# Performance work log

Hardware: AMD Instinct MI355X
Metric: run time of the kernel (lower is better)

## Reference

```python
import jax, jax.numpy as jnp
import numpy as np

B, E, H, L, V = 128, 1024, 1024, 2, 32001  # vocab = output_size + 1
PAD_IDX = 1000


def gru_cell(x, h, w_ih, w_hh, b_ih, b_hh):
    # PyTorch GRU cell math; gates ordered (r, z, n)
    gi = x @ w_ih.T + b_ih            # [B, 3H]
    gh = h @ w_hh.T + b_hh            # [B, 3H]
    i_r, i_z, i_n = jnp.split(gi, 3, axis=-1)
    h_r, h_z, h_n = jnp.split(gh, 3, axis=-1)
    r = jax.nn.sigmoid(i_r + h_r)
    z = jax.nn.sigmoid(i_z + h_z)
    n = jnp.tanh(i_n + r * h_n)
    return (1.0 - z) * n + z * h


def setup_inputs() -> dict:
    key = jax.random.key(0)
    ks = jax.random.split(key, 16)
    input_vector = jax.random.randint(ks[0], (B,), 0, V)
    hidden = jax.random.normal(ks[1], (L, B, H), dtype=jnp.float32)
    emb = jax.random.uniform(ks[2], (V, E), minval=-0.1, maxval=0.1, dtype=jnp.float32)
    emb = emb.at[PAD_IDX].set(0.0)  # padding_idx
    s = 1.0 / np.sqrt(H)
    def u(k, shape):
        return jax.random.uniform(k, shape, minval=-s, maxval=s, dtype=jnp.float32)
    w_ih0 = u(ks[3], (3 * H, E)); w_hh0 = u(ks[4], (3 * H, H))
    b_ih0 = u(ks[5], (3 * H,));  b_hh0 = u(ks[6], (3 * H,))
    w_ih1 = u(ks[7], (3 * H, H)); w_hh1 = u(ks[8], (3 * H, H))
    b_ih1 = u(ks[9], (3 * H,));  b_hh1 = u(ks[10], (3 * H,))
    w_out = jax.random.uniform(ks[11], (V, H), minval=-0.1, maxval=0.1, dtype=jnp.float32)
    b_out = jnp.zeros((V,), dtype=jnp.float32)
    return dict(input_vector=input_vector, hidden=hidden, emb=emb,
                w_ih0=w_ih0, w_hh0=w_hh0, b_ih0=b_ih0, b_hh0=b_hh0,
                w_ih1=w_ih1, w_hh1=w_hh1, b_ih1=b_ih1, b_hh1=b_hh1,
                w_out=w_out, b_out=b_out)


def reference(input_vector, hidden, emb, w_ih0, w_hh0, b_ih0, b_hh0,
              w_ih1, w_hh1, b_ih1, b_hh1, w_out, b_out):
    x = jax.nn.relu(emb[input_vector])          # [B, E] (seq_len=1 squeezed)
    h0 = gru_cell(x, hidden[0], w_ih0, w_hh0, b_ih0, b_hh0)   # [B, H]
    h1 = gru_cell(h0, hidden[1], w_ih1, w_hh1, b_ih1, b_hh1)  # [B, H]
    logits = h1 @ w_out.T + b_out               # [B, V]
    out = jax.nn.log_softmax(logits, axis=-1)   # [B, V]
    hidden_out = jnp.stack([h0, h1], axis=0)    # [L, B, H]
    return out, hidden_out
```

## Files before the change

kernel.cpp:

```cpp
#include <hip/hip_runtime.h>
#include <cmath>

#define BATCH 128
#define KDIM 1024
#define VOCAB 32001
#define G3 3072
#define GIP_STRIDE (BATCH * G3)

typedef __bf16 bf16_t;
typedef bf16_t bf16x8 __attribute__((ext_vector_type(8)));
typedef float f32x4 __attribute__((ext_vector_type(4)));

__device__ __forceinline__ void stage16(const void* g, void* lds) {
    __builtin_amdgcn_global_load_lds(
        (const __attribute__((address_space(1))) void*)g,
        (__attribute__((address_space(3))) void*)lds, 16, 0, 0);
}

template<bool BIAS>
__device__ __forceinline__ void gemm_core(
    const bf16_t* __restrict__ A, const float* __restrict__ W,
    const float* __restrict__ bias, float* __restrict__ C,
    int ldc, int Wrows, int n0, int kbeg, int kend)
{
    __shared__ bf16_t sA[2][128 * 64];
    __shared__ float  sB[2][64 * 64];
    const int t    = threadIdx.x;
    const int wave = t >> 6;
    const int lane = t & 63;
    const int l15  = lane & 15;
    const int quad = lane >> 4;
    const int wm   = wave & 1;
    const int wn   = wave >> 1;

    const bf16_t* aSrc[4]; int aDst[4];
#pragma unroll
    for (int r = 0; r < 4; ++r) {
        const int row = r * 32 + (t >> 3);
        const int sg  = t & 7;
        const int kg  = sg ^ (row & 7);
        aSrc[r] = A + (size_t)row * KDIM + kg * 8 + kbeg;
        aDst[r] = row * 128 + sg * 16;
    }
    const float* wSrc[4]; int wDst[4];
#pragma unroll
    for (int r = 0; r < 4; ++r) {
        const int row = r * 16 + (t >> 4);
        int wr = n0 + row; if (wr > Wrows - 1) wr = Wrows - 1;
        const int sg = t & 15;
        const int kg = sg ^ (row & 15);
        wSrc[r] = W + (size_t)wr * KDIM + kg * 4 + kbeg;
        wDst[r] = row * 256 + sg * 16;
    }

    f32x4 acc[4][2];
#pragma unroll
    for (int i = 0; i < 4; ++i)
#pragma unroll
        for (int j = 0; j < 2; ++j) acc[i][j] = f32x4{0.f, 0.f, 0.f, 0.f};

    const int nstages = (kend - kbeg) >> 6;

#pragma unroll
    for (int r = 0; r < 4; ++r) stage16(aSrc[r], (char*)sA[0] + aDst[r]);
#pragma unroll
    for (int r = 0; r < 4; ++r) stage16(wSrc[r], (char*)sB[0] + wDst[r]);
    __syncthreads();

    int cur = 0;
    for (int st = 0; st < nstages; ++st) {
        if (st + 1 < nstages) {
            const int off = (st + 1) << 6;
#pragma unroll
            for (int r = 0; r < 4; ++r) stage16(aSrc[r] + off, (char*)sA[cur ^ 1] + aDst[r]);
#pragma unroll
            for (int r = 0; r < 4; ++r) stage16(wSrc[r] + off, (char*)sB[cur ^ 1] + wDst[r]);
        }
        const char* sAc = (const char*)sA[cur];
        const char* sBc = (const char*)sB[cur];
#pragma unroll
        for (int s = 0; s < 2; ++s) {
            bf16x8 bfr[2];
#pragma unroll
            for (int j = 0; j < 2; ++j) {
                const int row = wn * 32 + j * 16 + l15;
                const int gu  = (s * 8 + 2 * quad) ^ (row & 15);
                const f32x4 u = *(const f32x4*)(sBc + row * 256 + gu * 16);
                const f32x4 v = *(const f32x4*)(sBc + row * 256 + (gu ^ 1) * 16);
                bf16x8 b;
                b[0] = (bf16_t)u[0]; b[1] = (bf16_t)u[1]; b[2] = (bf16_t)u[2]; b[3] = (bf16_t)u[3];
                b[4] = (bf16_t)v[0]; b[5] = (bf16_t)v[1]; b[6] = (bf16_t)v[2]; b[7] = (bf16_t)v[3];
                bfr[j] = b;
            }
#pragma unroll
            for (int i = 0; i < 4; ++i) {
                const int row  = wm * 64 + i * 16 + l15;
                const int phys = (s * 4 + quad) ^ (row & 7);
                const bf16x8 af = *(const bf16x8*)(sAc + row * 128 + phys * 16);
#pragma unroll
                for (int j = 0; j < 2; ++j)
                    acc[i][j] = __builtin_amdgcn_mfma_f32_16x16x32_bf16(
                        af, bfr[j], acc[i][j], 0, 0, 0);
            }
        }
        __syncthreads();
        cur ^= 1;
    }

#pragma unroll
    for (int j = 0; j < 2; ++j) {
        const int col = n0 + wn * 32 + j * 16 + l15;
        if (col < Wrows) {
            const float bv = BIAS ? bias[col] : 0.f;
#pragma unroll
            for (int i = 0; i < 4; ++i)
#pragma unroll
                for (int r = 0; r < 4; ++r) {
                    const int row = wm * 64 + i * 16 + quad * 4 + r;
                    C[(size_t)row * ldc + col] = acc[i][j][r] + bv;
                }
        }
    }
}

__global__ __launch_bounds__(256, 2) void gemm_gru(
    const bf16_t* __restrict__ Ai, const float* __restrict__ wih,
    float* __restrict__ giP,
    const bf16_t* __restrict__ Ah, const float* __restrict__ whh,
    float* __restrict__ ghP)
{
    const int split = blockIdx.x;
    const int n0    = blockIdx.y * 64;
    const int kbeg  = split * 256;
    if (blockIdx.z == 0)
        gemm_core<false>(Ai, wih, nullptr, giP + (size_t)split * GIP_STRIDE,
                         G3, G3, n0, kbeg, kbeg + 256);
    else
        gemm_core<false>(Ah, whh, nullptr, ghP + (size_t)split * GIP_STRIDE,
                         G3, G3, n0, kbeg, kbeg + 256);
}

__global__ __launch_bounds__(256, 2) void gemm_vocab(
    const bf16_t* __restrict__ A, const float* __restrict__ W,
    const float* __restrict__ bias, float* __restrict__ C)
{
    gemm_core<true>(A, W, bias, C, VOCAB, VOCAB, blockIdx.x * 64, 0, KDIM);
}

__global__ __launch_bounds__(256) void prep_bf16(const int* __restrict__ idx,
                                                 const float* __restrict__ emb,
                                                 const float* __restrict__ hidden,
                                                 bf16_t* __restrict__ dst) {
    const int i = blockIdx.x * 256 + threadIdx.x;
    const int sec = i >> 15;
    const int j   = i & 32767;
    f32x4 v;
    if (sec == 0) {
        const int b = j >> 8, e4 = j & 255;
        v = ((const f32x4*)(emb + (size_t)idx[b] * KDIM))[e4];
#pragma unroll
        for (int k = 0; k < 4; ++k) v[k] = fmaxf(v[k], 0.f);
    } else {
        v = ((const f32x4*)(hidden + (size_t)(sec - 1) * (BATCH * KDIM)))[j];
    }
    bf16_t o[4];
#pragma unroll
    for (int k = 0; k < 4; ++k) o[k] = (bf16_t)v[k];
    *(uint64_t*)(dst + (size_t)i * 4) = *(const uint64_t*)o;
}

__device__ __forceinline__ f32x4 sum_splits(const float* p) {
    f32x4 s = *(const f32x4*)p;
    s += *(const f32x4*)(p + GIP_STRIDE);
    s += *(const f32x4*)(p + 2 * GIP_STRIDE);
    s += *(const f32x4*)(p + 3 * GIP_STRIDE);
    return s;
}

__global__ __launch_bounds__(256) void gru_gate(const float* __restrict__ giP,
                                                const float* __restrict__ ghP,
                                                const float* __restrict__ b_ih,
                                                const float* __restrict__ b_hh,
                                                const float* __restrict__ hprev,
                                                float* __restrict__ hout,
                                                bf16_t* __restrict__ hout_bf16) {
    const int i  = blockIdx.x * 256 + threadIdx.x;
    const int b  = i >> 8;
    const int j  = (i & 255) * 4;
    const size_t base = (size_t)b * G3 + j;

    f32x4 ir = sum_splits(giP + base),        hr = sum_splits(ghP + base);
    f32x4 iz = sum_splits(giP + base + 1024), hz = sum_splits(ghP + base + 1024);
    f32x4 in = sum_splits(giP + base + 2048), hn = sum_splits(ghP + base + 2048);
    const f32x4 bir = *(const f32x4*)(b_ih + j);
    const f32x4 biz = *(const f32x4*)(b_ih + j + 1024);
    const f32x4 bin = *(const f32x4*)(b_ih + j + 2048);
    const f32x4 bhr = *(const f32x4*)(b_hh + j);
    const f32x4 bhz = *(const f32x4*)(b_hh + j + 1024);
    const f32x4 bhn = *(const f32x4*)(b_hh + j + 2048);
    const f32x4 hp  = *(const f32x4*)(hprev + (size_t)b * KDIM + j);

    f32x4 o;
    bf16_t ob[4];
#pragma unroll
    for (int k = 0; k < 4; ++k) {
        const float r = 1.f / (1.f + __expf(-(ir[k] + bir[k] + hr[k] + bhr[k])));
        const float z = 1.f / (1.f + __expf(-(iz[k] + biz[k] + hz[k] + bhz[k])));
        const float a = in[k] + bin[k] + r * (hn[k] + bhn[k]);
        const float n = 1.f - 2.f / (__expf(2.f * a) + 1.f);
        o[k] = (1.f - z) * n + z * hp[k];
        ob[k] = (bf16_t)o[k];
    }
    *(f32x4*)(hout + (size_t)b * KDIM + j) = o;
    *(uint64_t*)(hout_bf16 + (size_t)b * KDIM + j) = *(const uint64_t*)ob;
}

__global__ __launch_bounds__(1024) void log_softmax_rows(float* __restrict__ out) {
    float* row = out + (size_t)blockIdx.x * VOCAB;
    const int t = threadIdx.x;
    __shared__ float sm[16], ss[16];

    float m = -3.4e38f, s = 0.f;
    for (int i = t; i < VOCAB; i += 1024) {
        const float v  = row[i];
        const float mn = fmaxf(m, v);
        s = s * __expf(m - mn) + __expf(v - mn);
        m = mn;
    }
#pragma unroll
    for (int o = 32; o; o >>= 1) {
        const float mo = __shfl_down(m, o);
        const float so = __shfl_down(s, o);
        const float mn = fmaxf(m, mo);
        s = s * __expf(m - mn) + so * __expf(mo - mn);
        m = mn;
    }
    if ((t & 63) == 0) { sm[t >> 6] = m; ss[t >> 6] = s; }
    __syncthreads();
    if (t == 0) {
        float M = sm[0], S = ss[0];
#pragma unroll
        for (int w = 1; w < 16; ++w) {
            const float mn = fmaxf(M, sm[w]);
            S = S * __expf(M - mn) + ss[w] * __expf(sm[w] - mn);
            M = mn;
        }
        sm[0] = M + __logf(S);
    }
    __syncthreads();
    const float L = sm[0];

    for (int i = t * 4; i + 3 < VOCAB; i += 4096) {
        f32x4 v = *(const f32x4*)(row + i);
        v[0] -= L; v[1] -= L; v[2] -= L; v[3] -= L;
        *(f32x4*)(row + i) = v;
    }
    if (t == 0) row[32000] -= L;
}

extern "C" void kernel_launch(void* const* d_in, const int* in_sizes, int n_in,
                              void* d_out, int out_size, void* d_ws, size_t ws_size,
                              hipStream_t stream) {
    const int*   ivec  = (const int*)  d_in[0];
    const float* hidden= (const float*)d_in[1];
    const float* emb   = (const float*)d_in[2];
    const float* w_ih0 = (const float*)d_in[3];
    const float* w_hh0 = (const float*)d_in[4];
    const float* b_ih0 = (const float*)d_in[5];
    const float* b_hh0 = (const float*)d_in[6];
    const float* w_ih1 = (const float*)d_in[7];
    const float* w_hh1 = (const float*)d_in[8];
    const float* b_ih1 = (const float*)d_in[9];
    const float* b_hh1 = (const float*)d_in[10];
    const float* w_out = (const float*)d_in[11];
    const float* b_out = (const float*)d_in[12];

    float* out = (float*)d_out;
    float* h0  = out + (size_t)BATCH * VOCAB;
    float* h1  = h0 + BATCH * KDIM;

    float*  ws   = (float*)d_ws;
    float*  giP  = ws;
    float*  ghP  = ws + 4 * (size_t)GIP_STRIDE;
    bf16_t* xb   = (bf16_t*)(ws + 8 * (size_t)GIP_STRIDE);
    bf16_t* hp0b = xb   + BATCH * KDIM;
    bf16_t* hp1b = hp0b + BATCH * KDIM;
    bf16_t* h0b  = hp1b + BATCH * KDIM;
    bf16_t* h1b  = h0b  + BATCH * KDIM;

    const float* hprev0 = hidden;
    const float* hprev1 = hidden + BATCH * KDIM;

    prep_bf16<<<384, 256, 0, stream>>>(ivec, emb, hidden, xb);

    gemm_gru<<<dim3(4, 48, 2), 256, 0, stream>>>(xb, w_ih0, giP, hp0b, w_hh0, ghP);
    gru_gate<<<128, 256, 0, stream>>>(giP, ghP, b_ih0, b_hh0, hprev0, h0, h0b);

    gemm_gru<<<dim3(4, 48, 2), 256, 0, stream>>>(h0b, w_ih1, giP, hp1b, w_hh1, ghP);
    gru_gate<<<128, 256, 0, stream>>>(giP, ghP, b_ih1, b_hh1, hprev1, h1, h1b);

    gemm_vocab<<<501, 256, 0, stream>>>(h1b, w_out, b_out, out);

    log_softmax_rows<<<128, 1024, 0, stream>>>(out);
}
```

Measured before the change: 344.7 us.

## Fuse log-softmax into vocab GEMM via cooperative grid sync; hoist layer-1 hh GEMM

Hoists the layer-1 hidden-to-hidden GEMM, which depends only on the input hidden state, into the first GRU GEMM launch as a third z-slice, so it runs in parallel with layer-0 work. Replaces the vocab GEMM plus separate log-softmax kernel with one cooperative kernel. That kernel computes per-tile row max and sum in registers, reduces them across blocks using two grid syncs, and writes the normalized logits once, avoiding a full read-modify-write pass over the output. It also halves the gru_gate block size. The cost is cooperative-launch residency requirements (501 blocks must be co-resident) and grid-sync latency.

```diff
diff --git a/kernel.cpp b/kernel.cpp
--- a/kernel.cpp
+++ b/kernel.cpp
@@ -1,11 +1,15 @@
 #include <hip/hip_runtime.h>
+#include <hip/hip_cooperative_groups.h>
 #include <cmath>
+
+namespace cg = cooperative_groups;
 
 #define BATCH 128
 #define KDIM 1024
 #define VOCAB 32001
 #define G3 3072
 #define GIP_STRIDE (BATCH * G3)
+#define NEGF (-3.0e38f)
 
 typedef __bf16 bf16_t;
 typedef bf16_t bf16x8 __attribute__((ext_vector_type(8)));
@@ -60,7 +64,6 @@
         for (int j = 0; j < 2; ++j) acc[i][j] = f32x4{0.f, 0.f, 0.f, 0.f};
 
     const int nstages = (kend - kbeg) >> 6;
-
 #pragma unroll
     for (int r = 0; r < 4; ++r) stage16(aSrc[r], (char*)sA[0] + aDst[r]);
 #pragma unroll
@@ -123,28 +126,224 @@
     }
 }
 
-__global__ __launch_bounds__(256, 2) void gemm_gru(
-    const bf16_t* __restrict__ Ai, const float* __restrict__ wih,
-    float* __restrict__ giP,
-    const bf16_t* __restrict__ Ah, const float* __restrict__ whh,
-    float* __restrict__ ghP)
+__global__ __launch_bounds__(256, 2) void gemm_gru3(
+    const bf16_t* __restrict__ Abase, const float* __restrict__ w0,
+    const float* __restrict__ w1, const float* __restrict__ w2,
+    float* __restrict__ Pbase)
 {
     const int split = blockIdx.x;
     const int n0    = blockIdx.y * 64;
-    const int kbeg  = split * 256;
-    if (blockIdx.z == 0)
-        gemm_core<false>(Ai, wih, nullptr, giP + (size_t)split * GIP_STRIDE,
-                         G3, G3, n0, kbeg, kbeg + 256);
-    else
-        gemm_core<false>(Ah, whh, nullptr, ghP + (size_t)split * GIP_STRIDE,
-                         G3, G3, n0, kbeg, kbeg + 256);
-}
-
-__global__ __launch_bounds__(256, 2) void gemm_vocab(
+    const int z     = blockIdx.z;
+    const float* W  = (z == 0) ? w0 : ((z == 1) ? w1 : w2);
+    gemm_core<false>(Abase + (size_t)z * BATCH * KDIM, W, nullptr,
+                     Pbase + (size_t)z * 4 * GIP_STRIDE + (size_t)split * GIP_STRIDE,
+                     G3, G3, n0, split * 256, split * 256 + 256);
+}
+
+__global__ __launch_bounds__(256, 2) void gemm_gru1(
     const bf16_t* __restrict__ A, const float* __restrict__ W,
-    const float* __restrict__ bias, float* __restrict__ C)
+    float* __restrict__ P)
 {
-    gemm_core<true>(A, W, bias, C, VOCAB, VOCAB, blockIdx.x * 64, 0, KDIM);
+    const int split = blockIdx.x;
+    const int n0    = blockIdx.y * 64;
+    gemm_core<false>(A, W, nullptr, P + (size_t)split * GIP_STRIDE,
+                     G3, G3, n0, split * 256, split * 256 + 256);
+}
+
+__global__ __launch_bounds__(256, 2) void vocab_fused(
+    const bf16_t* __restrict__ A, const float* __restrict__ W,
+    const float* __restrict__ bias, float* __restrict__ C,
+    float* __restrict__ pm, float* __restrict__ ps, float* __restrict__ Lrow)
+{
+    __shared__ bf16_t sA[2][128 * 64];
+    __shared__ float  sB[2][64 * 64];
+    __shared__ float  sPm[2][128], sPs[2][128];
+    __shared__ float  sL[128];
+    __shared__ float  swm[4], sws[4];
+
+    const int bid  = blockIdx.x;
+    const int n0   = bid * 64;
+    const int t    = threadIdx.x;
+    const int wave = t >> 6;
+    const int lane = t & 63;
+    const int l15  = lane & 15;
+    const int quad = lane >> 4;
+    const int wm   = wave & 1;
+    const int wn   = wave >> 1;
+
+    const bf16_t* aSrc[4]; int aDst[4];
+#pragma unroll
+    for (int r = 0; r < 4; ++r) {
+        const int row = r * 32 + (t >> 3);
+        const int sg  = t & 7;
+        const int kg  = sg ^ (row & 7);
+        aSrc[r] = A + (size_t)row * KDIM + kg * 8;
+        aDst[r] = row * 128 + sg * 16;
+    }
+    const float* wSrc[4]; int wDst[4];
+#pragma unroll
+    for (int r = 0; r < 4; ++r) {
+        const int row = r * 16 + (t >> 4);
+        int wr = n0 + row; if (wr > VOCAB - 1) wr = VOCAB - 1;
+        const int sg = t & 15;
+        const int kg = sg ^ (row & 15);
+        wSrc[r] = W + (size_t)wr * KDIM + kg * 4;
+        wDst[r] = row * 256 + sg * 16;
+    }
+
+    f32x4 acc[4][2];
+#pragma unroll
+    for (int i = 0; i < 4; ++i)
+#pragma unroll
+        for (int j = 0; j < 2; ++j) acc[i][j] = f32x4{0.f, 0.f, 0.f, 0.f};
+
+#pragma unroll
+    for (int r = 0; r < 4; ++r) stage16(aSrc[r], (char*)sA[0] + aDst[r]);
+#pragma unroll
+    for (int r = 0; r < 4; ++r) stage16(wSrc[r], (char*)sB[0] + wDst[r]);
+    __syncthreads();
+
+    int cur = 0;
+    for (int st = 0; st < 16; ++st) {
+        if (st + 1 < 16) {
+            const int off = (st + 1) << 6;
+#pragma unroll
+            for (int r = 0; r < 4; ++r) stage16(aSrc[r] + off, (char*)sA[cur ^ 1] + aDst[r]);
+#pragma unroll
+            for (int r = 0; r < 4; ++r) stage16(wSrc[r] + off, (char*)sB[cur ^ 1] + wDst[r]);
+        }
+        const char* sAc = (const char*)sA[cur];
+        const char* sBc = (const char*)sB[cur];
+#pragma unroll
+        for (int s = 0; s < 2; ++s) {
+            bf16x8 bfr[2];
+#pragma unroll
+            for (int j = 0; j < 2; ++j) {
+                const int row = wn * 32 + j * 16 + l15;
+                const int gu  = (s * 8 + 2 * quad) ^ (row & 15);
+                const f32x4 u = *(const f32x4*)(sBc + row * 256 + gu * 16);
+                const f32x4 v = *(const f32x4*)(sBc + row * 256 + (gu ^ 1) * 16);
+                bf16x8 b;
+                b[0] = (bf16_t)u[0]; b[1] = (bf16_t)u[1]; b[2] = (bf16_t)u[2]; b[3] = (bf16_t)u[3];
+                b[4] = (bf16_t)v[0]; b[5] = (bf16_t)v[1]; b[6] = (bf16_t)v[2]; b[7] = (bf16_t)v[3];
+                bfr[j] = b;
+            }
+#pragma unroll
+            for (int i = 0; i < 4; ++i) {
+                const int row  = wm * 64 + i * 16 + l15;
+                const int phys = (s * 4 + quad) ^ (row & 7);
+                const bf16x8 af = *(const bf16x8*)(sAc + row * 128 + phys * 16);
+#pragma unroll
+                for (int j = 0; j < 2; ++j)
+                    acc[i][j] = __builtin_amdgcn_mfma_f32_16x16x32_bf16(
+                        af, bfr[j], acc[i][j], 0, 0, 0);
+            }
+        }
+        __syncthreads();
+        cur ^= 1;
+    }
+
+#pragma unroll
+    for (int j = 0; j < 2; ++j) {
+        int col = n0 + wn * 32 + j * 16 + l15;
+        const float bv = bias[col < VOCAB ? col : VOCAB - 1];
+#pragma unroll
+        for (int i = 0; i < 4; ++i)
+#pragma unroll
+            for (int r = 0; r < 4; ++r) acc[i][j][r] += bv;
+    }
+    {
+        const int col0 = n0 + wn * 32 + l15;
+        const bool ok0 = col0 < VOCAB, ok1 = (col0 + 16) < VOCAB;
+        float rm[4][4], rs[4][4];
+#pragma unroll
+        for (int i = 0; i < 4; ++i)
+#pragma unroll
+            for (int r = 0; r < 4; ++r) {
+                const float v0 = acc[i][0][r], v1 = acc[i][1][r];
+                float m = fmaxf(ok0 ? v0 : NEGF, ok1 ? v1 : NEGF);
+                float s = (ok0 ? __expf(v0 - m) : 0.f) + (ok1 ? __expf(v1 - m) : 0.f);
+#pragma unroll
+                for (int msk = 1; msk < 16; msk <<= 1) {
+                    const float mo = __shfl_xor(m, msk);
+                    const float so = __shfl_xor(s, msk);
+                    const float mn = fmaxf(m, mo);
+                    s = s * __expf(m - mn) + so * __expf(mo - mn);
+                    m = mn;
+                }
+                rm[i][r] = m; rs[i][r] = s;
+            }
+        if (l15 == 0) {
+#pragma unroll
+            for (int i = 0; i < 4; ++i)
+#pragma unroll
+                for (int r = 0; r < 4; ++r) {
+                    const int row = wm * 64 + i * 16 + quad * 4 + r;
+                    sPm[wn][row] = rm[i][r]; sPs[wn][row] = rs[i][r];
+                }
+        }
+    }
+    __syncthreads();
+    if (t < 128) {
+        const float m0 = sPm[0][t], s0 = sPs[0][t];
+        const float m1 = sPm[1][t], s1 = sPs[1][t];
+        const float mn = fmaxf(m0, m1);
+        const float ss = s0 * __expf(m0 - mn) + s1 * __expf(m1 - mn);
+        pm[(size_t)bid * 128 + t] = mn;
+        ps[(size_t)bid * 128 + t] = ss;
+    }
+    __threadfence();
+    cg::this_grid().sync();
+
+    if (bid < 128) {
+        const int row = bid;
+        float m = NEGF, s = 0.f;
+        for (int i = t; i < 501; i += 256) {
+            const float mo = pm[(size_t)i * 128 + row];
+            const float so = ps[(size_t)i * 128 + row];
+            const float mn = fmaxf(m, mo);
+            s = s * __expf(m - mn) + so * __expf(mo - mn);
+            m = mn;
+        }
+#pragma unroll
+        for (int o = 32; o; o >>= 1) {
+            const float mo = __shfl_down(m, o);
+            const float so = __shfl_down(s, o);
+            const float mn = fmaxf(m, mo);
+            s = s * __expf(m - mn) + so * __expf(mo - mn);
+            m = mn;
+        }
+        if ((t & 63) == 0) { swm[t >> 6] = m; sws[t >> 6] = s; }
+        __syncthreads();
+        if (t == 0) {
+            float M = swm[0], S = sws[0];
+#pragma unroll
+            for (int w = 1; w < 4; ++w) {
+                const float mn = fmaxf(M, swm[w]);
+                S = S * __expf(M - mn) + sws[w] * __expf(swm[w] - mn);
+                M = mn;
+            }
+            Lrow[row] = M + __logf(S);
+        }
+    }
+    __threadfence();
+    cg::this_grid().sync();
+
+    if (t < 128) sL[t] = Lrow[t];
+    __syncthreads();
+#pragma unroll
+    for (int j = 0; j < 2; ++j) {
+        const int col = n0 + wn * 32 + j * 16 + l15;
+        if (col < VOCAB) {
+#pragma unroll
+            for (int i = 0; i < 4; ++i)
+#pragma unroll
+                for (int r = 0; r < 4; ++r) {
+                    const int row = wm * 64 + i * 16 + quad * 4 + r;
+                    C[(size_t)row * VOCAB + col] = acc[i][j][r] - sL[row];
+                }
+        }
+    }
 }
 
 __global__ __launch_bounds__(256) void prep_bf16(const int* __restrict__ idx,
@@ -177,14 +376,14 @@
     return s;
 }
 
-__global__ __launch_bounds__(256) void gru_gate(const float* __restrict__ giP,
+__global__ __launch_bounds__(128) void gru_gate(const float* __restrict__ giP,
                                                 const float* __restrict__ ghP,
                                                 const float* __restrict__ b_ih,
                                                 const float* __restrict__ b_hh,
                                                 const float* __restrict__ hprev,
                                                 float* __restrict__ hout,
                                                 bf16_t* __restrict__ hout_bf16) {
-    const int i  = blockIdx.x * 256 + threadIdx.x;
+    const int i  = blockIdx.x * 128 + threadIdx.x;
     const int b  = i >> 8;
     const int j  = (i & 255) * 4;
     const size_t base = (size_t)b * G3 + j;
@@ -213,49 +412,6 @@
     }
     *(f32x4*)(hout + (size_t)b * KDIM + j) = o;
     *(uint64_t*)(hout_bf16 + (size_t)b * KDIM + j) = *(const uint64_t*)ob;
-}
-
-__global__ __launch_bounds__(1024) void log_softmax_rows(float* __restrict__ out) {
-    float* row = out + (size_t)blockIdx.x * VOCAB;
-    const int t = threadIdx.x;
-    __shared__ float sm[16], ss[16];
-
-    float m = -3.4e38f, s = 0.f;
-    for (int i = t; i < VOCAB; i += 1024) {
-        const float v  = row[i];
-        const float mn = fmaxf(m, v);
-        s = s * __expf(m - mn) + __expf(v - mn);
-        m = mn;
-    }
-#pragma unroll
-    for (int o = 32; o; o >>= 1) {
-        const float mo = __shfl_down(m, o);
-        const float so = __shfl_down(s, o);
-        const float mn = fmaxf(m, mo);
-        s = s * __expf(m - mn) + so * __expf(mo - mn);
-        m = mn;
-    }
-    if ((t & 63) == 0) { sm[t >> 6] = m; ss[t >> 6] = s; }
-    __syncthreads();
-    if (t == 0) {
-        float M = sm[0], S = ss[0];
-#pragma unroll
-        for (int w = 1; w < 16; ++w) {
-            const float mn = fmaxf(M, sm[w]);
-            S = S * __expf(M - mn) + ss[w] * __expf(sm[w] - mn);
-            M = mn;
-        }
-        sm[0] = M + __logf(S);
-    }
-    __syncthreads();
-    const float L = sm[0];
-
-    for (int i = t * 4; i + 3 < VOCAB; i += 4096) {
-        f32x4 v = *(const f32x4*)(row + i);
-        v[0] -= L; v[1] -= L; v[2] -= L; v[3] -= L;
-        *(f32x4*)(row + i) = v;
-    }
-    if (t == 0) row[32000] -= L;
 }
 
 extern "C" void kernel_launch(void* const* d_in, const int* in_sizes, int n_in,
@@ -279,27 +435,34 @@
     float* h0  = out + (size_t)BATCH * VOCAB;
     float* h1  = h0 + BATCH * KDIM;
 
-    float*  ws   = (float*)d_ws;
-    float*  giP  = ws;
-    float*  ghP  = ws + 4 * (size_t)GIP_STRIDE;
-    bf16_t* xb   = (bf16_t*)(ws + 8 * (size_t)GIP_STRIDE);
-    bf16_t* hp0b = xb   + BATCH * KDIM;
-    bf16_t* hp1b = hp0b + BATCH * KDIM;
-    bf16_t* h0b  = hp1b + BATCH * KDIM;
-    bf16_t* h1b  = h0b  + BATCH * KDIM;
-
-    const float* hprev0 = hidden;
-    const float* hprev1 = hidden + BATCH * KDIM;
+    float*  ws  = (float*)d_ws;
+    float*  P   = ws;
+    bf16_t* xb  = (bf16_t*)(ws + 12 * (size_t)GIP_STRIDE);
+    bf16_t* hp0b= xb   + BATCH * KDIM;
+    bf16_t* hp1b= hp0b + BATCH * KDIM;
+    bf16_t* h0b = hp1b + BATCH * KDIM;
+    bf16_t* h1b = h0b  + BATCH * KDIM;
+    float*  pm  = ws + 12 * (size_t)GIP_STRIDE + 5 * BATCH * KDIM / 2;
+    float*  ps_ = pm  + 501 * 128;
+    float*  Lr  = ps_ + 501 * 128;
+
+    (void)hp0b; (void)hp1b;
 
     prep_bf16<<<384, 256, 0, stream>>>(ivec, emb, hidden, xb);
 
-    gemm_gru<<<dim3(4, 48, 2), 256, 0, stream>>>(xb, w_ih0, giP, hp0b, w_hh0, ghP);
-    gru_gate<<<128, 256, 0, stream>>>(giP, ghP, b_ih0, b_hh0, hprev0, h0, h0b);
-
-    gemm_gru<<<dim3(4, 48, 2), 256, 0, stream>>>(h0b, w_ih1, giP, hp1b, w_hh1, ghP);
-    gru_gate<<<128, 256, 0, stream>>>(giP, ghP, b_ih1, b_hh1, hprev1, h1, h1b);
-
-    gemm_vocab<<<501, 256, 0, stream>>>(h1b, w_out, b_out, out);
-
-    log_softmax_rows<<<128, 1024, 0, stream>>>(out);
-}
+    gemm_gru3<<<dim3(4, 48, 3), 256, 0, stream>>>(xb, w_ih0, w_hh0, w_hh1, P);
+    gru_gate<<<256, 128, 0, stream>>>(P, P + 4 * (size_t)GIP_STRIDE,
+                                      b_ih0, b_hh0, hidden, h0, h0b);
+
+    gemm_gru1<<<dim3(4, 48), 256, 0, stream>>>(h0b, w_ih1, P);
+    gru_gate<<<256, 128, 0, stream>>>(P, P + 8 * (size_t)GIP_STRIDE,
+                                      b_ih1, b_hh1, hidden + BATCH * KDIM, h1, h1b);
+
+    {
+        const bf16_t* A_ = h1b; const float* W_ = w_out; const float* b_ = b_out;
+        float* C_ = out; float* pm_ = pm; float* ps2_ = ps_; float* L_ = Lr;
+        void* kargs[] = {&A_, &W_, &b_, &C_, &pm_, &ps2_, &L_};
+        hipLaunchCooperativeKernel((const void*)vocab_fused, dim3(501), dim3(256),
+                                   kargs, 0, stream);
+    }
+}
```

New measurement: 558.9 us. 62.1% more time.
